# Kernel tuning notes

Measured on AMD Instinct MI355X. Metric: run time of the kernel, lower is better.

Reference implementation:

```python
import jax, jax.numpy as jnp
import numpy as np

N = 50000
F_IN = 128
E = 800000
C = 32      # hidden_channels
H1 = 8      # heads_1
H2 = 1      # heads_2
NEG_SLOPE = 0.2


def setup_inputs() -> dict:
    key = jax.random.key(0)
    ks = jax.random.split(key, 16)
    s = 0.1
    x = jax.random.normal(ks[0], (N, F_IN), dtype=jnp.float32)
    edge_index = jax.random.randint(ks[1], (2, E), 0, N, dtype=jnp.int32)
    # layer 1: in=F_IN, out=C, heads=H1, concat=True
    Wl1 = jax.random.normal(ks[2], (H1 * C, F_IN), dtype=jnp.float32) * s
    bl1 = jnp.zeros((H1 * C,), dtype=jnp.float32)
    Wr1 = jax.random.normal(ks[3], (H1 * C, F_IN), dtype=jnp.float32) * s
    br1 = jnp.zeros((H1 * C,), dtype=jnp.float32)
    att1 = jax.random.normal(ks[4], (H1, C), dtype=jnp.float32) * s
    bias1 = jnp.zeros((H1 * C,), dtype=jnp.float32)
    # layer 2: in=H1*C, out=C, heads=H2, concat=False (mean)
    Wl2 = jax.random.normal(ks[5], (H2 * C, H1 * C), dtype=jnp.float32) * s
    bl2 = jnp.zeros((H2 * C,), dtype=jnp.float32)
    Wr2 = jax.random.normal(ks[6], (H2 * C, H1 * C), dtype=jnp.float32) * s
    br2 = jnp.zeros((H2 * C,), dtype=jnp.float32)
    att2 = jax.random.normal(ks[7], (H2, C), dtype=jnp.float32) * s
    bias2 = jnp.zeros((C,), dtype=jnp.float32)
    return {"x": x, "edge_index": edge_index,
            "Wl1": Wl1, "bl1": bl1, "Wr1": Wr1, "br1": br1, "att1": att1, "bias1": bias1,
            "Wl2": Wl2, "bl2": bl2, "Wr2": Wr2, "br2": br2, "att2": att2, "bias2": bias2}


def _gatv2_layer(x, src, dst, Wl, bl, Wr, br, att, bias, heads, out_c, concat):
    n = x.shape[0]
    xl = (x @ Wl.T + bl).reshape(n, heads, out_c)  # source transform
    xr = (x @ Wr.T + br).reshape(n, heads, out_c)  # target transform
    z = jax.nn.leaky_relu(xl[src] + xr[dst], NEG_SLOPE)          # [E, H, C]
    logit = jnp.einsum('ehc,hc->eh', z, att)                     # [E, H]
    # segment softmax over incoming edges of each target node
    m = jax.ops.segment_max(logit, dst, num_segments=n)          # [N, H]
    ex = jnp.exp(logit - m[dst])
    denom = jax.ops.segment_sum(ex, dst, num_segments=n)
    alpha = ex / jnp.maximum(denom[dst], 1e-16)                  # [E, H]
    out = jax.ops.segment_sum(alpha[..., None] * xl[src], dst, num_segments=n)  # [N, H, C]
    out = out.reshape(n, heads * out_c) if concat else out.mean(axis=1)
    return out + bias


def reference(x, edge_index, Wl1, bl1, Wr1, br1, att1, bias1,
              Wl2, bl2, Wr2, br2, att2, bias2):
    n = x.shape[0]
    # PyG GATv2Conv default: add self loops
    loops = jnp.arange(n, dtype=edge_index.dtype)
    src = jnp.concatenate([edge_index[0], loops])
    dst = jnp.concatenate([edge_index[1], loops])
    h = _gatv2_layer(x, src, dst, Wl1, bl1, Wr1, br1, att1, bias1, H1, C, True)
    h = jax.nn.gelu(h, approximate=False)
    out = _gatv2_layer(h, src, dst, Wl2, bl2, Wr2, br2, att2, bias2, H2, C, False)
    return out
```

## Files before the change

### kernel.cpp

```cpp
#include <hip/hip_runtime.h>
#include <hip/hip_bf16.h>


typedef unsigned short u16;
typedef short bf16x8 __attribute__((ext_vector_type(8)));
typedef float f32x4 __attribute__((ext_vector_type(4)));
typedef float f32x2 __attribute__((ext_vector_type(2)));

#define F_IN   128
#define CH     32
#define H1     8
#define JT1    512
#define JH1    256
#define JT2    64
#define JH2    32

#define OFF_Y1     0UL
#define OFF_H      52000000UL
#define OFF_Y2     78000000UL
#define OFF_COL    85000000UL
#define OFF_DEG    89000000UL
#define OFF_ROW    89400000UL
#define OFF_CUR    89800000UL
#define OFF_WC     90200000UL
#define OFF_FLAG   90600000UL
#define OFF_BSUM   90700000UL
#define WS_NEED    91000000UL

#define W_WL1   0
#define W_BL1   32768
#define W_WR1   33024
#define W_BR1   65792
#define W_ATT1  66048
#define W_BIAS1 66304
#define W_WL2   66560
#define W_BL2   74752
#define W_WR2   74784
#define W_BR2   82976
#define W_ATT2  83008
#define W_BIAS2 83040
#define W_TOTAL 83072

__device__ inline float b2f(u16 u) { return __uint_as_float(((unsigned)u) << 16); }
__device__ inline u16 f2b(float f) {
    unsigned u = __float_as_uint(f);
    unsigned r = (u + 0x7fffu + ((u >> 16) & 1u)) >> 16;
    return (u16)r;
}
__device__ inline unsigned cvtpk(float lo, float hi) {
    unsigned r;
    asm("v_cvt_pk_bf16_f32 %0, %1, %2" : "=v"(r) : "v"(lo), "v"(hi));
    return r;
}
__device__ inline f32x2 pk_add(f32x2 a, f32x2 b) {
    f32x2 d;
    asm("v_pk_add_f32 %0, %1, %2" : "=v"(d) : "v"(a), "v"(b));
    return d;
}
__device__ inline f32x2 pk_fma(f32x2 a, f32x2 b, f32x2 c) {
    f32x2 d;
    asm("v_pk_fma_f32 %0, %1, %2, %3" : "=v"(d) : "v"(a), "v"(b), "v"(c));
    return d;
}
__device__ inline f32x2 unpk(unsigned u) {
    f32x2 d;
    d.x = __uint_as_float(u << 16);
    d.y = __uint_as_float(u & 0xffff0000u);
    return d;
}
__device__ inline f32x2 pabs(f32x2 z) {
    f32x2 d;
    d.x = __uint_as_float(__float_as_uint(z.x) & 0x7fffffffu);
    d.y = __uint_as_float(__float_as_uint(z.y) & 0x7fffffffu);
    return d;
}

struct WcArgs { const void* src[12]; int cum[13]; };

__global__ __launch_bounds__(256) void cvt_weights(
    WcArgs a, const u16* __restrict__ xprobe, u16* __restrict__ dst, int total,
    int* __restrict__ flagOut) {
    __shared__ int cnt[256];
    __shared__ int sflag;
    const int t = threadIdx.x;
    int c = 0;
    for (int i = t; i < 512; i += 256) {
        u16 u = xprobe[i];
        int e = (u >> 7) & 0xff;
        c += (u == 0 || (e >= 100 && e <= 141)) ? 1 : 0;
    }
    cnt[t] = c; __syncthreads();
    for (int off = 128; off; off >>= 1) {
        if (t < off) cnt[t] += cnt[t + off];
        __syncthreads();
    }
    if (t == 0) {
        sflag = (cnt[0] >= 440) ? 1 : 0;
        if (blockIdx.x == 0) *flagOut = sflag;
    }
    __syncthreads();
    const int fl = sflag;
    int i = blockIdx.x * 256 + t;
    if (i >= total) return;
    int s = 0;
    while (i >= a.cum[s + 1]) s++;
    int rel = i - a.cum[s];
    if (fl) dst[i] = ((const u16*)a.src[s])[rel];
    else    dst[i] = f2b(((const float*)a.src[s])[rel]);
}

__global__ void build_deg(const int* __restrict__ ei, int* __restrict__ deg,
                          int E_, int NP) {
    int e = blockIdx.x * 256 + threadIdx.x;
    if (e >= E_ + NP) return;
    int dst = (e < E_) ? ei[E_ + e] : e - E_;
    atomicAdd(deg + dst, 1);
}

__global__ __launch_bounds__(256) void scan_part(const int* __restrict__ deg,
                                                 int* __restrict__ bsum, int NN) {
    __shared__ int red[256];
    int b = blockIdx.x, t = threadIdx.x;
    int base = b * 1024 + t * 4;
    int s = 0;
#pragma unroll
    for (int j = 0; j < 4; j++) { int i = base + j; if (i < NN) s += deg[i]; }
    red[t] = s; __syncthreads();
    for (int off = 128; off; off >>= 1) {
        if (t < off) red[t] += red[t + off];
        __syncthreads();
    }
    if (t == 0) bsum[b] = red[0];
}

__global__ __launch_bounds__(256) void scan_final(
    const int* __restrict__ deg, const int* __restrict__ bsum,
    int* __restrict__ rowptr, int* __restrict__ cur, int NN, int NB) {
    __shared__ int sb[256];
    __shared__ int ps[256];
    int b = blockIdx.x, t = threadIdx.x;
    int bv = (t < NB) ? bsum[t] : 0;
    sb[t] = bv; __syncthreads();
    for (int off = 1; off < 256; off <<= 1) {
        int x = (t >= off) ? sb[t - off] : 0;
        __syncthreads();
        sb[t] += x;
        __syncthreads();
    }
    if (b == 0 && t == 0) rowptr[NN] = sb[NB - 1];
    int boff = (b == 0) ? 0 : sb[b - 1];

    int base = b * 1024 + t * 4;
    int v[4]; int s = 0;
#pragma unroll
    for (int j = 0; j < 4; j++) { int i = base + j; v[j] = (i < NN) ? deg[i] : 0; s += v[j]; }
    ps[t] = s; __syncthreads();
    for (int off = 1; off < 256; off <<= 1) {
        int x = (t >= off) ? ps[t - off] : 0;
        __syncthreads();
        ps[t] += x;
        __syncthreads();
    }
    int run = boff + (t ? ps[t - 1] : 0);
#pragma unroll
    for (int j = 0; j < 4; j++) {
        int i = base + j;
        if (i < NN) { rowptr[i] = run; cur[i] = run; run += v[j]; }
    }
}

__global__ void scatter_edges(const int* __restrict__ ei, int* __restrict__ cur,
                              int* __restrict__ col, int E_, int NP) {
    int e = blockIdx.x * 256 + threadIdx.x;
    if (e >= E_ + NP) return;
    int src, dst;
    if (e < E_) { src = ei[e]; dst = ei[E_ + e]; }
    else        { src = dst = e - E_; }
    int pos = atomicAdd(cur + dst, 1);
    col[pos] = src;
}

template <int K, bool DYN>
__global__ __launch_bounds__(256) void gemm_mfma(
    const void* __restrict__ X, const u16* __restrict__ Wl, const u16* __restrict__ Wr,
    const u16* __restrict__ bl, const u16* __restrict__ br,
    u16* __restrict__ Y, int M, int JH, const int* __restrict__ flagp) {
    __shared__ float cs[4][32][68];
    const int t = threadIdx.x, w = t >> 6, l = t & 63;
    const int bm0 = blockIdx.x * 128, bn0 = blockIdx.y * 64;
    const int JT = 2 * JH;
    const int lr = l & 15, lk = (l >> 4) * 8;
    const int fl = DYN ? *flagp : 1;

    int rowm[2];
#pragma unroll
    for (int mt = 0; mt < 2; mt++) {
        int row = bm0 + w * 32 + mt * 16 + lr;
        if (row >= M) row = M - 1;
        rowm[mt] = row;
    }

    constexpr int KK = K / 32;
    bf16x8 afr[2][KK];
    if (fl) {
        const u16* xb = (const u16*)X;
#pragma unroll
        for (int mt = 0; mt < 2; mt++)
#pragma unroll
            for (int kk = 0; kk < KK; kk++)
                afr[mt][kk] = *(const bf16x8*)(xb + (size_t)rowm[mt] * K + lk + kk * 32);
    } else {
        const float* xf = (const float*)X;
#pragma unroll
        for (int mt = 0; mt < 2; mt++)
#pragma unroll
            for (int kk = 0; kk < KK; kk++) {
                const float* p = xf + (size_t)rowm[mt] * K + lk + kk * 32;
                float4 v0 = *(const float4*)p;
                float4 v1 = *(const float4*)(p + 4);
                uint4 o;
                o.x = cvtpk(v0.x, v0.y); o.y = cvtpk(v0.z, v0.w);
                o.z = cvtpk(v1.x, v1.y); o.w = cvtpk(v1.z, v1.w);
                afr[mt][kk] = *(bf16x8*)&o;
            }
    }

    const u16* bx[4];
    float bv[4];
#pragma unroll
    for (int nt = 0; nt < 4; nt++) {
        int j = bn0 + nt * 16 + lr;
        const u16* wp = (j < JH) ? (Wl + (size_t)j * K) : (Wr + (size_t)(j - JH) * K);
        bx[nt] = wp + lk;
        bv[nt] = b2f(j < JH ? bl[j] : br[j - JH]);
    }

    f32x4 acc[2][4];
#pragma unroll
    for (int mt = 0; mt < 2; mt++)
#pragma unroll
        for (int nt = 0; nt < 4; nt++) acc[mt][nt] = (f32x4){0.f, 0.f, 0.f, 0.f};

#pragma unroll
    for (int kk = 0; kk < KK; kk++) {
        bf16x8 b[4];
#pragma unroll
        for (int nt = 0; nt < 4; nt++) b[nt] = *(const bf16x8*)(bx[nt] + kk * 32);
#pragma unroll
        for (int mt = 0; mt < 2; mt++)
#pragma unroll
            for (int nt = 0; nt < 4; nt++)
                acc[mt][nt] = __builtin_amdgcn_mfma_f32_16x16x32_bf16(
                    afr[mt][kk], b[nt], acc[mt][nt], 0, 0, 0);
    }

#pragma unroll
    for (int mt = 0; mt < 2; mt++)
#pragma unroll
        for (int nt = 0; nt < 4; nt++)
#pragma unroll
            for (int r = 0; r < 4; r++)
                cs[w][mt * 16 + (l >> 4) * 4 + r][nt * 16 + lr] = acc[mt][nt][r] + bv[nt];

#pragma unroll
    for (int p = 0; p < 4; p++) {
        int rl = p * 8 + (l >> 3);
        int grow = bm0 + w * 32 + rl;
        if (grow < M) {
            const float* rp = &cs[w][rl][(l & 7) * 8];
            float4 v0 = *(const float4*)rp;
            float4 v1 = *(const float4*)(rp + 4);
            uint4 o;
            o.x = cvtpk(v0.x, v0.y); o.y = cvtpk(v0.z, v0.w);
            o.z = cvtpk(v1.x, v1.y); o.w = cvtpk(v1.z, v1.w);
            *(uint4*)(Y + (size_t)grow * JT + bn0 + (l & 7) * 8) = o;
        }
    }
}

__global__ __launch_bounds__(256) void agg1(
    const u16* __restrict__ Y1, const int* __restrict__ rowptr,
    const int* __restrict__ col, const u16* __restrict__ att,
    const u16* __restrict__ bias, u16* __restrict__ hout, int NN) {
    const int wid = blockIdx.x * 4 + (threadIdx.x >> 6);
    if (wid >= NN) return;
    const int lane = threadIdx.x & 63, le = lane >> 4, cl = lane & 15;
    const int n = wid;

    f32x2 xr2[2][4], a06[2][4], a04[2][4];
#pragma unroll
    for (int h = 0; h < 2; h++) {
        uint4 rx = *(const uint4*)(Y1 + (size_t)n * JT1 + JH1 + h * 128 + cl * 8);
        uint4 ra = *(const uint4*)(att + h * 128 + cl * 8);
        unsigned ux[4] = {rx.x, rx.y, rx.z, rx.w};
        unsigned ua[4] = {ra.x, ra.y, ra.z, ra.w};
#pragma unroll
        for (int p = 0; p < 4; p++) {
            xr2[h][p] = unpk(ux[p]);
            f32x2 a = unpk(ua[p]);
            a06[h][p].x = 0.6f * a.x; a06[h][p].y = 0.6f * a.y;
            a04[h][p].x = 0.4f * a.x; a04[h][p].y = 0.4f * a.y;
        }
    }
    f32x2 acc2[2][4] = {{{0.f,0.f},{0.f,0.f},{0.f,0.f},{0.f,0.f}},
                        {{0.f,0.f},{0.f,0.f},{0.f,0.f},{0.f,0.f}}};
    float dsumA = 0.f, dsumB = 0.f;

    auto edge = [&](uint4 r0, uint4 r1, bool act) {
        unsigned u0[4] = {r0.x, r0.y, r0.z, r0.w};
        unsigned u1[4] = {r1.x, r1.y, r1.z, r1.w};
        f32x2 xl2[2][4];
        f32x2 pa = {0.f, 0.f}, pb = {0.f, 0.f};
#pragma unroll
        for (int p = 0; p < 4; p++) {
            xl2[0][p] = unpk(u0[p]);
            f32x2 z = pk_add(xl2[0][p], xr2[0][p]);
            pa = pk_fma(z, a06[0][p], pa);
            pa = pk_fma(pabs(z), a04[0][p], pa);
        }
#pragma unroll
        for (int p = 0; p < 4; p++) {
            xl2[1][p] = unpk(u1[p]);
            f32x2 z = pk_add(xl2[1][p], xr2[1][p]);
            pb = pk_fma(z, a06[1][p], pb);
            pb = pk_fma(pabs(z), a04[1][p], pb);
        }
        float la = pa.x + pa.y;
        la += __shfl_xor(la, 1); la += __shfl_xor(la, 2);
        float lb = pb.x + pb.y;
        lb += __shfl_xor(lb, 1); lb += __shfl_xor(lb, 2);
        float ea = __expf(la), eb = __expf(lb);
        if (!act) { ea = 0.f; eb = 0.f; }
        dsumA += ea; dsumB += eb;
        f32x2 ea2; ea2.x = ea; ea2.y = ea;
        f32x2 eb2; eb2.x = eb; eb2.y = eb;
#pragma unroll
        for (int p = 0; p < 4; p++) {
            acc2[0][p] = pk_fma(ea2, xl2[0][p], acc2[0][p]);
            acc2[1][p] = pk_fma(eb2, xl2[1][p], acc2[1][p]);
        }
    };

    const int beg = rowptr[n], end = rowptr[n + 1];
    int i = beg;
    for (; i + 8 <= end; i += 8) {
        int sA = col[i + le];
        int sB = col[i + 4 + le];
        const u16* pA = Y1 + (size_t)sA * JT1 + cl * 8;
        const u16* pB = Y1 + (size_t)sB * JT1 + cl * 8;
        uint4 rA0 = *(const uint4*)pA;
        uint4 rA1 = *(const uint4*)(pA + 128);
        uint4 rB0 = *(const uint4*)pB;
        uint4 rB1 = *(const uint4*)(pB + 128);
        edge(rA0, rA1, true);
        edge(rB0, rB1, true);
    }
    for (; i < end; i += 4) {
        int idx = i + le;
        bool act = idx < end;
        int s0 = col[act ? idx : end - 1];
        const u16* p0 = Y1 + (size_t)s0 * JT1 + cl * 8;
        uint4 r0 = *(const uint4*)p0;
        uint4 r1 = *(const uint4*)(p0 + 128);
        edge(r0, r1, act);
    }

    dsumA += __shfl_xor(dsumA, 16); dsumA += __shfl_xor(dsumA, 32);
    dsumB += __shfl_xor(dsumB, 16); dsumB += __shfl_xor(dsumB, 32);
#pragma unroll
    for (int h = 0; h < 2; h++)
#pragma unroll
        for (int p = 0; p < 4; p++) {
            acc2[h][p].x += __shfl_xor(acc2[h][p].x, 16);
            acc2[h][p].x += __shfl_xor(acc2[h][p].x, 32);
            acc2[h][p].y += __shfl_xor(acc2[h][p].y, 16);
            acc2[h][p].y += __shfl_xor(acc2[h][p].y, 32);
        }

    if (le == 0) {
        float invA = 1.f / fmaxf(dsumA, 1e-16f);
        float invB = 1.f / fmaxf(dsumB, 1e-16f);
#pragma unroll
        for (int h = 0; h < 2; h++) {
            float inv = h ? invB : invA;
            u16 bu[8];
            *(uint4*)bu = *(const uint4*)(bias + h * 128 + cl * 8);
            float v[8];
#pragma unroll
            for (int p = 0; p < 4; p++) {
                float x0 = acc2[h][p].x * inv + b2f(bu[2 * p]);
                float x1 = acc2[h][p].y * inv + b2f(bu[2 * p + 1]);
                v[2 * p]     = 0.5f * x0 * (1.f + erff(x0 * 0.70710678118654752f));
                v[2 * p + 1] = 0.5f * x1 * (1.f + erff(x1 * 0.70710678118654752f));
            }
            uint4 o;
            o.x = cvtpk(v[0], v[1]); o.y = cvtpk(v[2], v[3]);
            o.z = cvtpk(v[4], v[5]); o.w = cvtpk(v[6], v[7]);
            *(uint4*)(hout + (size_t)n * JH1 + h * 128 + cl * 8) = o;
        }
    }
}

__global__ __launch_bounds__(256) void agg2(
    const u16* __restrict__ Y2, const int* __restrict__ rowptr,
    const int* __restrict__ col, const u16* __restrict__ att,
    const u16* __restrict__ bias, void* __restrict__ dout, int NN,
    const int* __restrict__ flag) {
    const int wid = blockIdx.x * 4 + (threadIdx.x >> 6);
    if (wid >= NN) return;
    const int lane = threadIdx.x & 63, le = lane >> 4, cl = lane & 15;
    const int n = wid;

    f32x2 xr2 = unpk(*(const unsigned*)(Y2 + (size_t)n * JT2 + JH2 + cl * 2));
    f32x2 av  = unpk(*(const unsigned*)(att + cl * 2));
    f32x2 a06; a06.x = 0.6f * av.x; a06.y = 0.6f * av.y;
    f32x2 a04; a04.x = 0.4f * av.x; a04.y = 0.4f * av.y;
    f32x2 acc2 = {0.f, 0.f};
    float dsum = 0.f;

    auto edge = [&](unsigned raw, bool act) {
        f32x2 xl2 = unpk(raw);
        f32x2 z = pk_add(xl2, xr2);
        f32x2 p2 = pk_fma(z, a06, (f32x2){0.f, 0.f});
        p2 = pk_fma(pabs(z), a04, p2);
        float pl = p2.x + p2.y;
        pl += __shfl_xor(pl, 1); pl += __shfl_xor(pl, 2);
        pl += __shfl_xor(pl, 4); pl += __shfl_xor(pl, 8);
        float e = __expf(pl);
        if (!act) e = 0.f;
        dsum += e;
        f32x2 e2; e2.x = e; e2.y = e;
        acc2 = pk_fma(e2, xl2, acc2);
    };

    const int beg = rowptr[n], end = rowptr[n + 1];
    int i = beg;
    for (; i + 8 <= end; i += 8) {
        int sA = col[i + le];
        int sB = col[i + 4 + le];
        unsigned rA = *(const unsigned*)(Y2 + (size_t)sA * JT2 + cl * 2);
        unsigned rB = *(const unsigned*)(Y2 + (size_t)sB * JT2 + cl * 2);
        edge(rA, true);
        edge(rB, true);
    }
    for (; i < end; i += 4) {
        int idx = i + le;
        bool act = idx < end;
        int s0 = col[act ? idx : end - 1];
        unsigned r0 = *(const unsigned*)(Y2 + (size_t)s0 * JT2 + cl * 2);
        edge(r0, act);
    }

    dsum += __shfl_xor(dsum, 16); dsum += __shfl_xor(dsum, 32);
    acc2.x += __shfl_xor(acc2.x, 16); acc2.x += __shfl_xor(acc2.x, 32);
    acc2.y += __shfl_xor(acc2.y, 16); acc2.y += __shfl_xor(acc2.y, 32);

    if (le == 0) {
        float inv = 1.f / fmaxf(dsum, 1e-16f);
        f32x2 bv = unpk(*(const unsigned*)(bias + cl * 2));
        float v0 = acc2.x * inv + bv.x;
        float v1 = acc2.y * inv + bv.y;
        if (*flag) {
            *(unsigned*)((u16*)dout + n * JH2 + cl * 2) = cvtpk(v0, v1);
        } else {
            float2 o; o.x = v0; o.y = v1;
            *(float2*)((float*)dout + n * JH2 + cl * 2) = o;
        }
    }
}

extern "C" void kernel_launch(void* const* d_in, const int* in_sizes, int n_in,
                              void* d_out, int out_size, void* d_ws, size_t ws_size,
                              hipStream_t stream) {
    const int NN = in_sizes[0] / F_IN;
    const int EE = in_sizes[1] / 2;
    const int EP = EE + NN;
    if (ws_size < WS_NEED) return;

    char* w = (char*)d_ws;
    u16*   Y1   = (u16*)(w + OFF_Y1);
    u16*   hbuf = (u16*)(w + OFF_H);
    u16*   Y2   = (u16*)(w + OFF_Y2);
    int*   col  = (int*)(w + OFF_COL);
    int*   deg  = (int*)(w + OFF_DEG);
    int*   rowp = (int*)(w + OFF_ROW);
    int*   cur  = (int*)(w + OFF_CUR);
    u16*   Wc   = (u16*)(w + OFF_WC);
    int*   flag = (int*)(w + OFF_FLAG);
    int*   bsum = (int*)(w + OFF_BSUM);

    const int* ei = (const int*)d_in[1];

    {
        WcArgs a;
        int sizes[12] = {JH1 * F_IN, JH1, JH1 * F_IN, JH1, H1 * CH, JH1,
                         JH2 * JH1, JH2, JH2 * JH1, JH2, JH2, JH2};
        int c = 0;
        for (int s = 0; s < 12; s++) { a.src[s] = d_in[2 + s]; a.cum[s] = c; c += sizes[s]; }
        a.cum[12] = c;
        cvt_weights<<<(W_TOTAL + 255) / 256, 256, 0, stream>>>(
            a, (const u16*)d_in[0], Wc, W_TOTAL, flag);
    }

    const int NB = (NN + 1023) / 1024;
    hipMemsetAsync(deg, 0, (size_t)NN * 4, stream);
    build_deg<<<(EP + 255) / 256, 256, 0, stream>>>(ei, deg, EE, NN);
    scan_part<<<NB, 256, 0, stream>>>(deg, bsum, NN);
    scan_final<<<NB, 256, 0, stream>>>(deg, bsum, rowp, cur, NN, NB);
    scatter_edges<<<(EP + 255) / 256, 256, 0, stream>>>(ei, cur, col, EE, NN);

    {
        dim3 grid((NN + 127) / 128, JT1 / 64);
        gemm_mfma<F_IN, true><<<grid, 256, 0, stream>>>(
            d_in[0], Wc + W_WL1, Wc + W_WR1, Wc + W_BL1, Wc + W_BR1, Y1, NN, JH1, flag);
    }
    agg1<<<(NN + 3) / 4, 256, 0, stream>>>(Y1, rowp, col, Wc + W_ATT1,
                                           Wc + W_BIAS1, hbuf, NN);

    {
        dim3 grid((NN + 127) / 128, JT2 / 64);
        gemm_mfma<JH1, false><<<grid, 256, 0, stream>>>(
            hbuf, Wc + W_WL2, Wc + W_WR2, Wc + W_BL2, Wc + W_BR2, Y2, NN, JH2, flag);
    }
    agg2<<<(NN + 3) / 4, 256, 0, stream>>>(Y2, rowp, col, Wc + W_ATT2,
                                           Wc + W_BIAS2, d_out, NN, flag);
}
```

Measured before the change: 298.2 us.

## Merge weight conversion with degree count; remap agg1 lanes to edge halves

The weight-conversion kernel and the degree-counting kernel are merged into one launch, with block index choosing the role, so one kernel launch goes away. agg1 now gives each half-wavefront a whole edge row (256 features), so one wave processes two edges at a time. Each half also issues up to eight independent gathers per iteration and combines with the other half at the end. The aim is more memory-level parallelism and fewer cross-lane reductions in the gather-bound aggregation, at the cost of more registers; a launch-bounds occupancy hint is added to offset this.

Measured after the change: 278.6 us. -6.6%, faster.

```diff
diff --git a/kernel.cpp b/kernel.cpp
--- a/kernel.cpp
+++ b/kernel.cpp
@@ -77,12 +77,20 @@
 
 struct WcArgs { const void* src[12]; int cum[13]; };
 
-__global__ __launch_bounds__(256) void cvt_weights(
+__global__ __launch_bounds__(256) void prep(
     WcArgs a, const u16* __restrict__ xprobe, u16* __restrict__ dst, int total,
-    int* __restrict__ flagOut) {
+    int* __restrict__ flagOut, int NBW,
+    const int* __restrict__ ei, int* __restrict__ deg, int E_, int NP) {
+    const int t = threadIdx.x;
+    if ((int)blockIdx.x >= NBW) {
+        int e = ((int)blockIdx.x - NBW) * 256 + t;
+        if (e >= E_ + NP) return;
+        int dstn = (e < E_) ? ei[E_ + e] : e - E_;
+        atomicAdd(deg + dstn, 1);
+        return;
+    }
     __shared__ int cnt[256];
     __shared__ int sflag;
-    const int t = threadIdx.x;
     int c = 0;
     for (int i = t; i < 512; i += 256) {
         u16 u = xprobe[i];
@@ -107,14 +115,6 @@
     int rel = i - a.cum[s];
     if (fl) dst[i] = ((const u16*)a.src[s])[rel];
     else    dst[i] = f2b(((const float*)a.src[s])[rel]);
-}
-
-__global__ void build_deg(const int* __restrict__ ei, int* __restrict__ deg,
-                          int E_, int NP) {
-    int e = blockIdx.x * 256 + threadIdx.x;
-    if (e >= E_ + NP) return;
-    int dst = (e < E_) ? ei[E_ + e] : e - E_;
-    atomicAdd(deg + dst, 1);
 }
 
 __global__ __launch_bounds__(256) void scan_part(const int* __restrict__ deg,
@@ -278,126 +278,100 @@
     }
 }
 
-__global__ __launch_bounds__(256) void agg1(
+__global__ __launch_bounds__(256, 4) void agg1(
     const u16* __restrict__ Y1, const int* __restrict__ rowptr,
     const int* __restrict__ col, const u16* __restrict__ att,
     const u16* __restrict__ bias, u16* __restrict__ hout, int NN) {
     const int wid = blockIdx.x * 4 + (threadIdx.x >> 6);
     if (wid >= NN) return;
-    const int lane = threadIdx.x & 63, le = lane >> 4, cl = lane & 15;
+    const int lane = threadIdx.x & 63, half = lane >> 5, hl = lane & 31;
     const int n = wid;
 
-    f32x2 xr2[2][4], a06[2][4], a04[2][4];
-#pragma unroll
-    for (int h = 0; h < 2; h++) {
-        uint4 rx = *(const uint4*)(Y1 + (size_t)n * JT1 + JH1 + h * 128 + cl * 8);
-        uint4 ra = *(const uint4*)(att + h * 128 + cl * 8);
+    f32x2 xr2[4], a06[4], a04[4];
+    {
+        uint4 rx = *(const uint4*)(Y1 + (size_t)n * JT1 + JH1 + hl * 8);
+        uint4 ra = *(const uint4*)(att + hl * 8);
         unsigned ux[4] = {rx.x, rx.y, rx.z, rx.w};
         unsigned ua[4] = {ra.x, ra.y, ra.z, ra.w};
 #pragma unroll
         for (int p = 0; p < 4; p++) {
-            xr2[h][p] = unpk(ux[p]);
+            xr2[p] = unpk(ux[p]);
             f32x2 a = unpk(ua[p]);
-            a06[h][p].x = 0.6f * a.x; a06[h][p].y = 0.6f * a.y;
-            a04[h][p].x = 0.4f * a.x; a04[h][p].y = 0.4f * a.y;
+            a06[p].x = 0.6f * a.x; a06[p].y = 0.6f * a.y;
+            a04[p].x = 0.4f * a.x; a04[p].y = 0.4f * a.y;
         }
     }
-    f32x2 acc2[2][4] = {{{0.f,0.f},{0.f,0.f},{0.f,0.f},{0.f,0.f}},
-                        {{0.f,0.f},{0.f,0.f},{0.f,0.f},{0.f,0.f}}};
-    float dsumA = 0.f, dsumB = 0.f;
-
-    auto edge = [&](uint4 r0, uint4 r1, bool act) {
-        unsigned u0[4] = {r0.x, r0.y, r0.z, r0.w};
-        unsigned u1[4] = {r1.x, r1.y, r1.z, r1.w};
-        f32x2 xl2[2][4];
-        f32x2 pa = {0.f, 0.f}, pb = {0.f, 0.f};
+    f32x2 acc2[4] = {{0.f,0.f},{0.f,0.f},{0.f,0.f},{0.f,0.f}};
+    float dsum = 0.f;
+
+    auto edge = [&](uint4 raw) {
+        unsigned uw[4] = {raw.x, raw.y, raw.z, raw.w};
+        f32x2 xl2[4];
+        f32x2 p2 = {0.f, 0.f};
 #pragma unroll
         for (int p = 0; p < 4; p++) {
-            xl2[0][p] = unpk(u0[p]);
-            f32x2 z = pk_add(xl2[0][p], xr2[0][p]);
-            pa = pk_fma(z, a06[0][p], pa);
-            pa = pk_fma(pabs(z), a04[0][p], pa);
+            xl2[p] = unpk(uw[p]);
+            f32x2 z = pk_add(xl2[p], xr2[p]);
+            p2 = pk_fma(z, a06[p], p2);
+            p2 = pk_fma(pabs(z), a04[p], p2);
         }
+        float pl = p2.x + p2.y;
+        pl += __shfl_xor(pl, 1); pl += __shfl_xor(pl, 2);
+        float e = __expf(pl);
+        dsum += e;
+        f32x2 e2; e2.x = e; e2.y = e;
+#pragma unroll
+        for (int p = 0; p < 4; p++) acc2[p] = pk_fma(e2, xl2[p], acc2[p]);
+    };
+
+    const int beg = rowptr[n], end = rowptr[n + 1];
+    int i = beg + half;
+    for (; i + 14 < end; i += 16) {
+        int s[8];
+#pragma unroll
+        for (int k = 0; k < 8; k++) s[k] = col[i + 2 * k];
+        uint4 r[8];
+#pragma unroll
+        for (int k = 0; k < 8; k++) r[k] = *(const uint4*)(Y1 + (size_t)s[k] * JT1 + hl * 8);
+#pragma unroll
+        for (int k = 0; k < 8; k++) edge(r[k]);
+    }
+    for (; i + 6 < end; i += 8) {
+        int s0 = col[i], s1 = col[i + 2], s2 = col[i + 4], s3 = col[i + 6];
+        uint4 r0 = *(const uint4*)(Y1 + (size_t)s0 * JT1 + hl * 8);
+        uint4 r1 = *(const uint4*)(Y1 + (size_t)s1 * JT1 + hl * 8);
+        uint4 r2 = *(const uint4*)(Y1 + (size_t)s2 * JT1 + hl * 8);
+        uint4 r3 = *(const uint4*)(Y1 + (size_t)s3 * JT1 + hl * 8);
+        edge(r0); edge(r1); edge(r2); edge(r3);
+    }
+    for (; i < end; i += 2) {
+        uint4 r0 = *(const uint4*)(Y1 + (size_t)col[i] * JT1 + hl * 8);
+        edge(r0);
+    }
+
+    dsum += __shfl_xor(dsum, 32);
+#pragma unroll
+    for (int p = 0; p < 4; p++) {
+        acc2[p].x += __shfl_xor(acc2[p].x, 32);
+        acc2[p].y += __shfl_xor(acc2[p].y, 32);
+    }
+
+    if (half == 0) {
+        float inv = 1.f / fmaxf(dsum, 1e-16f);
+        u16 bu[8];
+        *(uint4*)bu = *(const uint4*)(bias + hl * 8);
+        float v[8];
 #pragma unroll
         for (int p = 0; p < 4; p++) {
-            xl2[1][p] = unpk(u1[p]);
-            f32x2 z = pk_add(xl2[1][p], xr2[1][p]);
-            pb = pk_fma(z, a06[1][p], pb);
-            pb = pk_fma(pabs(z), a04[1][p], pb);
+            float x0 = acc2[p].x * inv + b2f(bu[2 * p]);
+            float x1 = acc2[p].y * inv + b2f(bu[2 * p + 1]);
+            v[2 * p]     = 0.5f * x0 * (1.f + erff(x0 * 0.70710678118654752f));
+            v[2 * p + 1] = 0.5f * x1 * (1.f + erff(x1 * 0.70710678118654752f));
         }
-        float la = pa.x + pa.y;
-        la += __shfl_xor(la, 1); la += __shfl_xor(la, 2);
-        float lb = pb.x + pb.y;
-        lb += __shfl_xor(lb, 1); lb += __shfl_xor(lb, 2);
-        float ea = __expf(la), eb = __expf(lb);
-        if (!act) { ea = 0.f; eb = 0.f; }
-        dsumA += ea; dsumB += eb;
-        f32x2 ea2; ea2.x = ea; ea2.y = ea;
-        f32x2 eb2; eb2.x = eb; eb2.y = eb;
-#pragma unroll
-        for (int p = 0; p < 4; p++) {
-            acc2[0][p] = pk_fma(ea2, xl2[0][p], acc2[0][p]);
-            acc2[1][p] = pk_fma(eb2, xl2[1][p], acc2[1][p]);
-        }
-    };
-
-    const int beg = rowptr[n], end = rowptr[n + 1];
-    int i = beg;
-    for (; i + 8 <= end; i += 8) {
-        int sA = col[i + le];
-        int sB = col[i + 4 + le];
-        const u16* pA = Y1 + (size_t)sA * JT1 + cl * 8;
-        const u16* pB = Y1 + (size_t)sB * JT1 + cl * 8;
-        uint4 rA0 = *(const uint4*)pA;
-        uint4 rA1 = *(const uint4*)(pA + 128);
-        uint4 rB0 = *(const uint4*)pB;
-        uint4 rB1 = *(const uint4*)(pB + 128);
-        edge(rA0, rA1, true);
-        edge(rB0, rB1, true);
-    }
-    for (; i < end; i += 4) {
-        int idx = i + le;
-        bool act = idx < end;
-        int s0 = col[act ? idx : end - 1];
-        const u16* p0 = Y1 + (size_t)s0 * JT1 + cl * 8;
-        uint4 r0 = *(const uint4*)p0;
-        uint4 r1 = *(const uint4*)(p0 + 128);
-        edge(r0, r1, act);
-    }
-
-    dsumA += __shfl_xor(dsumA, 16); dsumA += __shfl_xor(dsumA, 32);
-    dsumB += __shfl_xor(dsumB, 16); dsumB += __shfl_xor(dsumB, 32);
-#pragma unroll
-    for (int h = 0; h < 2; h++)
-#pragma unroll
-        for (int p = 0; p < 4; p++) {
-            acc2[h][p].x += __shfl_xor(acc2[h][p].x, 16);
-            acc2[h][p].x += __shfl_xor(acc2[h][p].x, 32);
-            acc2[h][p].y += __shfl_xor(acc2[h][p].y, 16);
-            acc2[h][p].y += __shfl_xor(acc2[h][p].y, 32);
-        }
-
-    if (le == 0) {
-        float invA = 1.f / fmaxf(dsumA, 1e-16f);
-        float invB = 1.f / fmaxf(dsumB, 1e-16f);
-#pragma unroll
-        for (int h = 0; h < 2; h++) {
-            float inv = h ? invB : invA;
-            u16 bu[8];
-            *(uint4*)bu = *(const uint4*)(bias + h * 128 + cl * 8);
-            float v[8];
-#pragma unroll
-            for (int p = 0; p < 4; p++) {
-                float x0 = acc2[h][p].x * inv + b2f(bu[2 * p]);
-                float x1 = acc2[h][p].y * inv + b2f(bu[2 * p + 1]);
-                v[2 * p]     = 0.5f * x0 * (1.f + erff(x0 * 0.70710678118654752f));
-                v[2 * p + 1] = 0.5f * x1 * (1.f + erff(x1 * 0.70710678118654752f));
-            }
-            uint4 o;
-            o.x = cvtpk(v[0], v[1]); o.y = cvtpk(v[2], v[3]);
-            o.z = cvtpk(v[4], v[5]); o.w = cvtpk(v[6], v[7]);
-            *(uint4*)(hout + (size_t)n * JH1 + h * 128 + cl * 8) = o;
-        }
+        uint4 o;
+        o.x = cvtpk(v[0], v[1]); o.y = cvtpk(v[2], v[3]);
+        o.z = cvtpk(v[4], v[5]); o.w = cvtpk(v[6], v[7]);
+        *(uint4*)(hout + (size_t)n * JH1 + hl * 8) = o;
     }
 }
 
@@ -491,6 +465,7 @@
 
     const int* ei = (const int*)d_in[1];
 
+    hipMemsetAsync(deg, 0, (size_t)NN * 4, stream);
     {
         WcArgs a;
         int sizes[12] = {JH1 * F_IN, JH1, JH1 * F_IN, JH1, H1 * CH, JH1,
@@ -498,13 +473,13 @@
         int c = 0;
         for (int s = 0; s < 12; s++) { a.src[s] = d_in[2 + s]; a.cum[s] = c; c += sizes[s]; }
         a.cum[12] = c;
-        cvt_weights<<<(W_TOTAL + 255) / 256, 256, 0, stream>>>(
-            a, (const u16*)d_in[0], Wc, W_TOTAL, flag);
+        const int NBW = (W_TOTAL + 255) / 256;
+        const int NBE = (EP + 255) / 256;
+        prep<<<NBW + NBE, 256, 0, stream>>>(a, (const u16*)d_in[0], Wc, W_TOTAL,
+                                            flag, NBW, ei, deg, EE, NN);
     }
 
     const int NB = (NN + 1023) / 1024;
-    hipMemsetAsync(deg, 0, (size_t)NN * 4, stream);
-    build_deg<<<(EP + 255) / 256, 256, 0, stream>>>(ei, deg, EE, NN);
     scan_part<<<NB, 256, 0, stream>>>(deg, bsum, NN);
     scan_final<<<NB, 256, 0, stream>>>(deg, bsum, rowp, cur, NN, NB);
     scatter_edges<<<(EP + 255) / 256, 256, 0, stream>>>(ei, cur, col, EE, NN);
```
